# Kernel optimization log

Hardware: AMD Instinct MI355X
Metric: run time of the kernel (lower is better)

The kernel has to match this reference:

```python
import math
import jax, jax.numpy as jnp
import numpy as np

B, L, H = 32, 1024, 128

def setup_inputs() -> dict:
    key = jax.random.key(0)
    k1, k2, k3, k4 = jax.random.split(key, 4)
    a = jax.random.normal(k1, (B, L, H), dtype=jnp.float32)
    b = jax.random.normal(k2, (B, L, H), dtype=jnp.float32)
    mask_a = jax.random.randint(k3, (B, L, 1), 0, 2, dtype=jnp.int32)
    mask_b = jax.random.randint(k4, (B, L, 1), 0, 2, dtype=jnp.int32)
    temperature = jnp.asarray(1.0 / math.sqrt(H), dtype=jnp.float32)
    return {"a": a, "b": b, "mask_a": mask_a, "mask_b": mask_b, "temperature": temperature}

def reference(a, b, mask_a, mask_b, temperature):
    # scores: [B, La, Lb]
    scores = jnp.einsum('bld,bmd->blm', a, b) * temperature
    # outer product of token validity masks -> pair mask [B, La, Lb]
    mask = jnp.einsum('blk,bmk->blm', mask_a.astype(jnp.float32), mask_b.astype(jnp.float32)) > 0
    scores = jnp.where(mask, scores, jnp.float32(-10000.0))
    attention_a = jax.nn.softmax(scores, axis=1)  # normalize over La (columns)
    attention_b = jax.nn.softmax(scores, axis=2)  # normalize over Lb (rows)
    feature_a = jnp.einsum('blm,bmd->bld', attention_b, b)
    feature_b = jnp.einsum('blm,bmd->bld', attention_a, a)  # valid since La == Lb
    return (feature_a, feature_b)
```

## Files before the change

kernel.cpp:

```cpp
#include <hip/hip_runtime.h>
#include <math.h>

#define BN 32
#define LL 1024
#define HH 128

typedef __attribute__((ext_vector_type(8))) short short8;
typedef __attribute__((ext_vector_type(4))) float f32x4;

static const size_t SZ_BF = (size_t)BN * LL * HH * 2;

__device__ __forceinline__ ushort f2bf(float x) {
  union { float f; unsigned u; } c; c.f = x;
  unsigned r = c.u + 0x7fffu + ((c.u >> 16) & 1u);
  return (ushort)(r >> 16);
}
__device__ __forceinline__ float bf2f(ushort h) {
  union { unsigned u; float f; } c; c.u = ((unsigned)h) << 16;
  return c.f;
}
__device__ __forceinline__ short8 ld8(const ushort* p) {
  return *(const short8*)p;
}

__global__ __launch_bounds__(256) void k_convert(
    const float* __restrict__ a, const float* __restrict__ b,
    const int* __restrict__ mask_b,
    ushort* __restrict__ abf, ushort* __restrict__ bbf,
    ushort* __restrict__ aT, ushort* __restrict__ bT,
    float* __restrict__ meanb, float* __restrict__ invmean) {
  int bb = blockIdx.y;
  int l0 = blockIdx.x * 64;
  int which = blockIdx.z;
  const float* src = which ? b : a;
  ushort* dst  = which ? bbf : abf;
  ushort* dstT = which ? bT : aT;
  float* dmean = which ? meanb : invmean;
  __shared__ __align__(16) ushort T[128][72];
  __shared__ float accS[128];
  __shared__ float wgt[64];
  int t = threadIdx.x;
  if (t < 128) accS[t] = 0.f;
  if (t < 64)
    wgt[t] = which ? 1.0f : ((mask_b[bb * LL + l0 + t] == 0) ? 1.0f : 0.0f);
  int lrow = t >> 5;
  int dcol = (t & 31) * 4;
#pragma unroll
  for (int p = 0; p < 8; ++p) {
    int l = p * 8 + lrow;
    float4 v = *(const float4*)&src[((size_t)bb * LL + l0 + l) * HH + dcol];
    ushort4 u;
    u.x = f2bf(v.x); u.y = f2bf(v.y); u.z = f2bf(v.z); u.w = f2bf(v.w);
    *(ushort4*)&dst[((size_t)bb * LL + l0 + l) * HH + dcol] = u;
    T[dcol + 0][l] = u.x; T[dcol + 1][l] = u.y;
    T[dcol + 2][l] = u.z; T[dcol + 3][l] = u.w;
  }
  __syncthreads();
  int drow = t >> 3;
  int c8 = (t & 7) * 8;
#pragma unroll
  for (int q = 0; q < 4; ++q) {
    int d = q * 32 + drow;
    short8 val = *(const short8*)&T[d][c8];
    *(short8*)&dstT[((size_t)bb * HH + d) * LL + l0 + c8] = val;
    float s = 0.f;
#pragma unroll
    for (int j = 0; j < 8; ++j) s += wgt[c8 + j] * bf2f((ushort)val[j]);
    atomicAdd(&accS[d], s);
  }
  __syncthreads();
  if (t < 128) atomicAdd(&dmean[bb * HH + t], accS[t]);
}


__global__ __launch_bounds__(256, 2) void k_colsum(
    const ushort* __restrict__ abf, const ushort* __restrict__ bbf,
    ushort* __restrict__ aTm,
    const int* __restrict__ mask_a, const int* __restrict__ mask_b,
    const float* __restrict__ temp_p, float2* __restrict__ cc) {
  int wg = blockIdx.x;
  int xcd = wg & 7, k_ = wg >> 3;
  int bb = (k_ >> 4) * 8 + xcd;
  int m0 = (k_ & 15) * 64;
  int t = threadIdx.x;
  int w = t >> 6, lane = t & 63, l16 = lane & 15, quad = lane >> 4;
  float temp = temp_p[0];
  __shared__ __align__(16) float biasA[LL];
  __shared__ float csred[4][4][16];
  __shared__ float invS[64];
  for (int i = t; i < LL; i += 256)
    biasA[i] = mask_a[bb * LL + i] ? 0.0f : -10000.0f;

  short8 Bm[4][4];
  float biasB_mt[4];
#pragma unroll
  for (int mt = 0; mt < 4; ++mt) {
    int m = m0 + mt * 16 + l16;
    biasB_mt[mt] = mask_b[bb * LL + m] ? 0.0f : -10000.0f;
#pragma unroll
    for (int k = 0; k < 4; ++k)
      Bm[mt][k] = ld8(&bbf[((size_t)bb * LL + m) * HH + k * 32 + quad * 8]);
  }
  __syncthreads();

  float cs[4] = {0.f, 0.f, 0.f, 0.f};
  short8 Al0[4], Al1[4];

#define LOADAL(AlX, IT)                                                       \
  {                                                                           \
    const ushort* arow = &abf[((size_t)bb * LL + w * 256 + (IT) * 16 + l16) * HH]; \
    _Pragma("unroll") for (int k = 0; k < 4; ++k)                             \
        AlX[k] = ld8(&arow[k * 32 + quad * 8]);                               \
  }

#define CSCOMPUTE(AlX, IT)                                                    \
  {                                                                           \
    int lbase = w * 256 + (IT) * 16;                                          \
    f32x4 bA = *(const f32x4*)&biasA[lbase + quad * 4];                       \
    _Pragma("unroll") for (int mt = 0; mt < 4; ++mt) {                        \
      f32x4 sacc = {0.f, 0.f, 0.f, 0.f};                                      \
      _Pragma("unroll") for (int k = 0; k < 4; ++k)                           \
          sacc = __builtin_amdgcn_mfma_f32_16x16x32_bf16(AlX[k], Bm[mt][k],   \
                                                         sacc, 0, 0, 0);      \
      _Pragma("unroll") for (int r = 0; r < 4; ++r)                           \
          cs[mt] += __expf(sacc[r] * temp + bA[r] + biasB_mt[mt]);            \
    }                                                                         \
  }

  LOADAL(Al0, 0);
  for (int it = 0; it < 16; it += 2) {
    LOADAL(Al1, it + 1);
    CSCOMPUTE(Al0, it);
    LOADAL(Al0, (it + 2) & 15);
    CSCOMPUTE(Al1, it + 1);
  }
#undef LOADAL
#undef CSCOMPUTE

#pragma unroll
  for (int mt = 0; mt < 4; ++mt) {
    cs[mt] += __shfl_xor(cs[mt], 16);
    cs[mt] += __shfl_xor(cs[mt], 32);
  }
  if (lane < 16) {
#pragma unroll
    for (int mt = 0; mt < 4; ++mt) csred[w][mt][l16] = cs[mt];
  }
  __syncthreads();
  if (t < 64) {
    int mt = t >> 4, ml = t & 15;
    float s = csred[0][mt][ml] + csred[1][mt][ml] + csred[2][mt][ml] + csred[3][mt][ml];
    int m = m0 + t;
    float bB = mask_b[bb * LL + m] ? 0.0f : -10000.0f;
    float inv = s > 0.f ? 1.0f / s : 0.0f;
    invS[t] = inv;
    cc[bb * LL + m] = make_float2(inv, bB);
  }
  __syncthreads();

  {
    int d = t >> 1, mc = (t & 1) * 32;
    ushort* ap = &aTm[((size_t)bb * HH + d) * LL + m0 + mc];
    short8 v0 = ld8(ap), v1 = ld8(ap + 8), v2 = ld8(ap + 16), v3 = ld8(ap + 24);
    ushort o[32];
#pragma unroll
    for (int j = 0; j < 8; ++j) {
      o[j]      = f2bf(bf2f((ushort)v0[j]) * invS[mc + j]);
      o[8 + j]  = f2bf(bf2f((ushort)v1[j]) * invS[mc + 8 + j]);
      o[16 + j] = f2bf(bf2f((ushort)v2[j]) * invS[mc + 16 + j]);
      o[24 + j] = f2bf(bf2f((ushort)v3[j]) * invS[mc + 24 + j]);
    }
    *(short8*)ap        = *(short8*)&o[0];
    *(short8*)(ap + 8)  = *(short8*)&o[8];
    *(short8*)(ap + 16) = *(short8*)&o[16];
    *(short8*)(ap + 24) = *(short8*)&o[24];
  }
}

__global__ __launch_bounds__(256, 2) void k_features(
    const ushort* __restrict__ abf, const ushort* __restrict__ bbf,
    const ushort* __restrict__ aT, const ushort* __restrict__ bT,
    const int* __restrict__ mask_a, const float* __restrict__ temp_p,
    const float2* __restrict__ cc, const float* __restrict__ meanb,
    const float* __restrict__ invmean, float* __restrict__ out) {
  int wg = blockIdx.x;
  int xcd = wg & 7, k_ = wg >> 3;
  int bb = (k_ >> 4) * 8 + xcd;
  int l0 = (k_ & 15) * 64;
  int t = threadIdx.x;
  int w = t >> 6, lane = t & 63, l16 = lane & 15, quad = lane >> 4;
  float temp = temp_p[0];

  __shared__ float2 ccs[LL];
  __shared__ __align__(16) ushort Pa[2][64 * 72];
  __shared__ float rspart[4][64];
  __shared__ float rsfin[64];

  for (int i = t; i < LL; i += 256) ccs[i] = cc[bb * LL + i];

  float biasA_lt[4];
  short8 Afix[4][4];
#pragma unroll
  for (int lt = 0; lt < 4; ++lt) {
    int l = l0 + lt * 16 + l16;
    biasA_lt[lt] = mask_a[bb * LL + l] ? 0.0f : -10000.0f;
#pragma unroll
    for (int k = 0; k < 4; ++k)
      Afix[lt][k] = ld8(&abf[((size_t)bb * LL + l) * HH + k * 32 + quad * 8]);
  }

  f32x4 accA[4][2], accB[4][2];
  f32x4 zero = {0.f, 0.f, 0.f, 0.f};
#pragma unroll
  for (int lt = 0; lt < 4; ++lt)
#pragma unroll
    for (int dt = 0; dt < 2; ++dt) { accA[lt][dt] = zero; accB[lt][dt] = zero; }
  float rs_lt[4] = {0.f, 0.f, 0.f, 0.f};
  __syncthreads();

  short8 Am0[4], Am1[4];
  float cv0[4], cv1[4];
  short8 Bb0[2][2], Ba0[2][2], Bb1[2][2], Ba1[2][2];

#define LOADAM(AmX, cvX, M0)                                                  \
  {                                                                           \
    const ushort* brow = &bbf[((size_t)bb * LL + (M0) + w * 16 + l16) * HH];  \
    _Pragma("unroll") for (int k = 0; k < 4; ++k)                             \
        AmX[k] = ld8(&brow[k * 32 + quad * 8]);                               \
    _Pragma("unroll") for (int r = 0; r < 4; ++r)                             \
        cvX[r] = ccs[(M0) + w * 16 + quad * 4 + r].y;                         \
  }

#define LOADBT(BbX, BaX, M0)                                                  \
  {                                                                           \
    _Pragma("unroll") for (int dt = 0; dt < 2; ++dt) {                        \
      const ushort* btrow =                                                   \
          &bT[((size_t)bb * HH + w * 32 + dt * 16 + l16) * LL + (M0)];        \
      const ushort* atrow =                                                   \
          &aT[((size_t)bb * HH + w * 32 + dt * 16 + l16) * LL + (M0)];        \
      _Pragma("unroll") for (int ks = 0; ks < 2; ++ks) {                      \
        BbX[dt][ks] = ld8(&btrow[ks * 32 + quad * 8]);                        \
        BaX[dt][ks] = ld8(&atrow[ks * 32 + quad * 8]);                        \
      }                                                                       \
    }                                                                         \
  }

#define SPHASE(AmX, cvX, PBUFI)                                               \
  {                                                                           \
    ushort* pa = &Pa[PBUFI][0];                                               \
    _Pragma("unroll") for (int lt = 0; lt < 4; ++lt) {                        \
      f32x4 sacc = zero;                                                      \
      _Pragma("unroll") for (int k = 0; k < 4; ++k)                           \
          sacc = __builtin_amdgcn_mfma_f32_16x16x32_bf16(AmX[k], Afix[lt][k], \
                                                         sacc, 0, 0, 0);      \
      ushort pav[4];                                                          \
      _Pragma("unroll") for (int r = 0; r < 4; ++r) {                         \
        float e = __expf(sacc[r] * temp + biasA_lt[lt] + cvX[r]);             \
        pav[r] = f2bf(e);                                                     \
        rs_lt[lt] += bf2f(pav[r]);                                            \
      }                                                                       \
      uint2 ka;                                                               \
      ka.x = (uint)pav[0] | ((uint)pav[1] << 16);                             \
      ka.y = (uint)pav[2] | ((uint)pav[3] << 16);                             \
      int pidx = (lt * 16 + l16) * 72 + w * 16 + quad * 4;                    \
      *(uint2*)&pa[pidx] = ka;                                                \
    }                                                                         \
  }

#define FPHASE(PBUFI, BbX, BaX)                                               \
  {                                                                           \
    const ushort* pa = &Pa[PBUFI][0];                                         \
    _Pragma("unroll") for (int lt = 0; lt < 4; ++lt) {                        \
      _Pragma("unroll") for (int ks = 0; ks < 2; ++ks) {                      \
        int ridx = (lt * 16 + l16) * 72 + ks * 32 + quad * 8;                 \
        short8 PaF = *(const short8*)&pa[ridx];                               \
        _Pragma("unroll") for (int dt = 0; dt < 2; ++dt) {                    \
          accA[lt][dt] = __builtin_amdgcn_mfma_f32_16x16x32_bf16(             \
              PaF, BbX[dt][ks], accA[lt][dt], 0, 0, 0);                       \
          accB[lt][dt] = __builtin_amdgcn_mfma_f32_16x16x32_bf16(             \
              PaF, BaX[dt][ks], accB[lt][dt], 0, 0, 0);                       \
        }                                                                     \
      }                                                                       \
    }                                                                         \
  }

  LOADAM(Am0, cv0, 0);
  LOADBT(Bb0, Ba0, 0);
  LOADAM(Am1, cv1, 64);
  SPHASE(Am0, cv0, 0);
  __syncthreads();

  for (int kk = 0; kk < 7; ++kk) {
    int mA = (2 * kk + 1) * 64;
    LOADBT(Bb1, Ba1, mA);
    LOADAM(Am0, cv0, mA + 64);
    SPHASE(Am1, cv1, 1);
    FPHASE(0, Bb0, Ba0);
    __syncthreads();
    LOADBT(Bb0, Ba0, mA + 64);
    LOADAM(Am1, cv1, mA + 128);
    SPHASE(Am0, cv0, 0);
    FPHASE(1, Bb1, Ba1);
    __syncthreads();
  }

  LOADBT(Bb1, Ba1, 960);
  SPHASE(Am1, cv1, 1);
  FPHASE(0, Bb0, Ba0);
  __syncthreads();
  FPHASE(1, Bb1, Ba1);

#undef LOADAM
#undef LOADBT
#undef SPHASE
#undef FPHASE

#pragma unroll
  for (int lt = 0; lt < 4; ++lt) {
    rs_lt[lt] += __shfl_xor(rs_lt[lt], 16);
    rs_lt[lt] += __shfl_xor(rs_lt[lt], 32);
  }
  if (lane < 16) {
#pragma unroll
    for (int lt = 0; lt < 4; ++lt) rspart[w][lt * 16 + l16] = rs_lt[lt];
  }
  __syncthreads();
  if (t < 64)
    rsfin[t] = rspart[0][t] + rspart[1][t] + rspart[2][t] + rspart[3][t];
  __syncthreads();

  float* outA = out;
  float* outB = out + (size_t)BN * LL * HH;
#pragma unroll
  for (int dt = 0; dt < 2; ++dt) {
    int d = w * 32 + dt * 16 + l16;
    float mb = meanb[bb * HH + d] * (1.0f / 1024.0f);
    float im = invmean[bb * HH + d] * (1.0f / 1024.0f);
#pragma unroll
    for (int lt = 0; lt < 4; ++lt) {
#pragma unroll
      for (int r = 0; r < 4; ++r) {
        int l = lt * 16 + quad * 4 + r;
        float rsv = rsfin[l];
        float fa = (rsv > 0.f) ? accA[lt][dt][r] / rsv : mb;
        float fb = accB[lt][dt][r] + im;
        __builtin_nontemporal_store(fa, &outA[((size_t)bb * LL + l0 + l) * HH + d]);
        __builtin_nontemporal_store(fb, &outB[((size_t)bb * LL + l0 + l) * HH + d]);
      }
    }
  }
}

extern "C" void kernel_launch(void* const* d_in, const int* in_sizes, int n_in,
                              void* d_out, int out_size, void* d_ws, size_t ws_size,
                              hipStream_t stream) {
  const float* a = (const float*)d_in[0];
  const float* b = (const float*)d_in[1];
  const int* mask_a = (const int*)d_in[2];
  const int* mask_b = (const int*)d_in[3];
  const float* temp = (const float*)d_in[4];
  float* out = (float*)d_out;

  char* wsb = (char*)d_ws;
  ushort* abf = (ushort*)(wsb + 0 * SZ_BF);
  ushort* bbf = (ushort*)(wsb + 1 * SZ_BF);
  ushort* aT  = (ushort*)(wsb + 2 * SZ_BF);
  ushort* bT  = (ushort*)(wsb + 3 * SZ_BF);
  float2* cc  = (float2*)(wsb + 4 * SZ_BF);
  float* meanb   = (float*)(wsb + 4 * SZ_BF + (size_t)BN * LL * sizeof(float2));
  float* invmean = meanb + BN * HH;

  hipMemsetAsync(meanb, 0, 2 * BN * HH * sizeof(float), stream);
  k_convert<<<dim3(16, 32, 2), 256, 0, stream>>>(a, b, mask_b, abf, bbf, aT, bT,
                                                 meanb, invmean);
  k_colsum<<<dim3(512), 256, 0, stream>>>(abf, bbf, aT, mask_a, mask_b, temp, cc);
  k_features<<<dim3(512), 256, 0, stream>>>(abf, bbf, aT, bT, mask_a, temp,
                                            cc, meanb, invmean, out);
  (void)in_sizes; (void)n_in; (void)out_size; (void)ws_size;
}
```

Baseline: 203.8 us.

## Pre-swizzle bf16 operands into MFMA fragment-contiguous chunks

```diff
diff --git a/kernel.cpp b/kernel.cpp
--- a/kernel.cpp
+++ b/kernel.cpp
@@ -23,18 +23,25 @@
   return *(const short8*)p;
 }
 
+__device__ __forceinline__ size_t chunkS(int bb, int g, int k) {
+  return (((size_t)bb * 64 + g) * 4 + k) * 512;
+}
+__device__ __forceinline__ size_t chunkT(int bb, int dg, int mb) {
+  return (((size_t)bb * 8 + dg) * 32 + mb) * 512;
+}
+
 __global__ __launch_bounds__(256) void k_convert(
     const float* __restrict__ a, const float* __restrict__ b,
     const int* __restrict__ mask_b,
-    ushort* __restrict__ abf, ushort* __restrict__ bbf,
-    ushort* __restrict__ aT, ushort* __restrict__ bT,
+    ushort* __restrict__ abfs, ushort* __restrict__ bbfs,
+    ushort* __restrict__ aTs, ushort* __restrict__ bTs,
     float* __restrict__ meanb, float* __restrict__ invmean) {
   int bb = blockIdx.y;
   int l0 = blockIdx.x * 64;
   int which = blockIdx.z;
   const float* src = which ? b : a;
-  ushort* dst  = which ? bbf : abf;
-  ushort* dstT = which ? bT : aT;
+  ushort* dstS = which ? bbfs : abfs;
+  ushort* dstT = which ? bTs : aTs;
   float* dmean = which ? meanb : invmean;
   __shared__ __align__(16) ushort T[128][72];
   __shared__ float accS[128];
@@ -51,22 +58,28 @@
     float4 v = *(const float4*)&src[((size_t)bb * LL + l0 + l) * HH + dcol];
     ushort4 u;
     u.x = f2bf(v.x); u.y = f2bf(v.y); u.z = f2bf(v.z); u.w = f2bf(v.w);
-    *(ushort4*)&dst[((size_t)bb * LL + l0 + l) * HH + dcol] = u;
+    int g = (l0 >> 4) + (l >> 4);
+    int k = dcol >> 5, quadc = (dcol >> 3) & 3, j = dcol & 7;
+    *(ushort4*)&dstS[chunkS(bb, g, k) + (size_t)(quadc * 16 + (l & 15)) * 8 + j] = u;
     T[dcol + 0][l] = u.x; T[dcol + 1][l] = u.y;
     T[dcol + 2][l] = u.z; T[dcol + 3][l] = u.w;
   }
   __syncthreads();
-  int drow = t >> 3;
-  int c8 = (t & 7) * 8;
-#pragma unroll
-  for (int q = 0; q < 4; ++q) {
-    int d = q * 32 + drow;
-    short8 val = *(const short8*)&T[d][c8];
-    *(short8*)&dstT[((size_t)bb * HH + d) * LL + l0 + c8] = val;
+#pragma unroll
+  for (int c = 0; c < 4; ++c) {
+    int cid = c * 4 + (t >> 6);
+    int dg = cid >> 1, mloc = cid & 1;
+    int lane = t & 63, l16c = lane & 15, qc = lane >> 4;
+    int row = dg * 16 + l16c, colb = mloc * 32 + qc * 8;
+    uint2 vlo = *(const uint2*)&T[row][colb];
+    uint2 vhi = *(const uint2*)&T[row][colb + 4];
+    union { uint4 u4; short8 s8; ushort us[8]; } cv_;
+    cv_.u4 = make_uint4(vlo.x, vlo.y, vhi.x, vhi.y);
+    *(short8*)&dstT[chunkT(bb, dg, (l0 >> 5) + mloc) + (size_t)lane * 8] = cv_.s8;
     float s = 0.f;
 #pragma unroll
-    for (int j = 0; j < 8; ++j) s += wgt[c8 + j] * bf2f((ushort)val[j]);
-    atomicAdd(&accS[d], s);
+    for (int jj = 0; jj < 8; ++jj) s += wgt[colb + jj] * bf2f(cv_.us[jj]);
+    atomicAdd(&accS[row], s);
   }
   __syncthreads();
   if (t < 128) atomicAdd(&dmean[bb * HH + t], accS[t]);
@@ -74,7 +87,7 @@
 
 
 __global__ __launch_bounds__(256, 2) void k_colsum(
-    const ushort* __restrict__ abf, const ushort* __restrict__ bbf,
+    const ushort* __restrict__ abfs, const ushort* __restrict__ bbfs,
     ushort* __restrict__ aTm,
     const int* __restrict__ mask_a, const int* __restrict__ mask_b,
     const float* __restrict__ temp_p, float2* __restrict__ cc) {
@@ -99,7 +112,7 @@
     biasB_mt[mt] = mask_b[bb * LL + m] ? 0.0f : -10000.0f;
 #pragma unroll
     for (int k = 0; k < 4; ++k)
-      Bm[mt][k] = ld8(&bbf[((size_t)bb * LL + m) * HH + k * 32 + quad * 8]);
+      Bm[mt][k] = ld8(&bbfs[chunkS(bb, (m0 >> 4) + mt, k) + (size_t)lane * 8]);
   }
   __syncthreads();
 
@@ -108,9 +121,8 @@
 
 #define LOADAL(AlX, IT)                                                       \
   {                                                                           \
-    const ushort* arow = &abf[((size_t)bb * LL + w * 256 + (IT) * 16 + l16) * HH]; \
     _Pragma("unroll") for (int k = 0; k < 4; ++k)                             \
-        AlX[k] = ld8(&arow[k * 32 + quad * 8]);                               \
+        AlX[k] = ld8(&abfs[chunkS(bb, w * 16 + (IT), k) + (size_t)lane * 8]); \
   }
 
 #define CSCOMPUTE(AlX, IT)                                                    \
@@ -158,28 +170,24 @@
   }
   __syncthreads();
 
-  {
-    int d = t >> 1, mc = (t & 1) * 32;
-    ushort* ap = &aTm[((size_t)bb * HH + d) * LL + m0 + mc];
-    short8 v0 = ld8(ap), v1 = ld8(ap + 8), v2 = ld8(ap + 16), v3 = ld8(ap + 24);
-    ushort o[32];
-#pragma unroll
-    for (int j = 0; j < 8; ++j) {
-      o[j]      = f2bf(bf2f((ushort)v0[j]) * invS[mc + j]);
-      o[8 + j]  = f2bf(bf2f((ushort)v1[j]) * invS[mc + 8 + j]);
-      o[16 + j] = f2bf(bf2f((ushort)v2[j]) * invS[mc + 16 + j]);
-      o[24 + j] = f2bf(bf2f((ushort)v3[j]) * invS[mc + 24 + j]);
-    }
-    *(short8*)ap        = *(short8*)&o[0];
-    *(short8*)(ap + 8)  = *(short8*)&o[8];
-    *(short8*)(ap + 16) = *(short8*)&o[16];
-    *(short8*)(ap + 24) = *(short8*)&o[24];
+#pragma unroll
+  for (int q = 0; q < 4; ++q) {
+    int cid = q * 4 + (t >> 6);
+    int dg = cid >> 1, mloc = cid & 1;
+    int ln = t & 63;
+    ushort* ap = &aTm[chunkT(bb, dg, (m0 >> 5) + mloc) + (size_t)ln * 8];
+    short8 v = ld8(ap);
+    int mb = mloc * 32 + (ln >> 4) * 8;
+    ushort o[8];
+#pragma unroll
+    for (int j = 0; j < 8; ++j) o[j] = f2bf(bf2f((ushort)v[j]) * invS[mb + j]);
+    *(short8*)ap = *(short8*)&o[0];
   }
 }
 
 __global__ __launch_bounds__(256, 2) void k_features(
-    const ushort* __restrict__ abf, const ushort* __restrict__ bbf,
-    const ushort* __restrict__ aT, const ushort* __restrict__ bT,
+    const ushort* __restrict__ abfs, const ushort* __restrict__ bbfs,
+    const ushort* __restrict__ aTs, const ushort* __restrict__ bTs,
     const int* __restrict__ mask_a, const float* __restrict__ temp_p,
     const float2* __restrict__ cc, const float* __restrict__ meanb,
     const float* __restrict__ invmean, float* __restrict__ out) {
@@ -206,7 +214,7 @@
     biasA_lt[lt] = mask_a[bb * LL + l] ? 0.0f : -10000.0f;
 #pragma unroll
     for (int k = 0; k < 4; ++k)
-      Afix[lt][k] = ld8(&abf[((size_t)bb * LL + l) * HH + k * 32 + quad * 8]);
+      Afix[lt][k] = ld8(&abfs[chunkS(bb, (l0 >> 4) + lt, k) + (size_t)lane * 8]);
   }
 
   f32x4 accA[4][2], accB[4][2];
@@ -224,9 +232,8 @@
 
 #define LOADAM(AmX, cvX, M0)                                                  \
   {                                                                           \
-    const ushort* brow = &bbf[((size_t)bb * LL + (M0) + w * 16 + l16) * HH];  \
     _Pragma("unroll") for (int k = 0; k < 4; ++k)                             \
-        AmX[k] = ld8(&brow[k * 32 + quad * 8]);                               \
+        AmX[k] = ld8(&bbfs[chunkS(bb, ((M0) >> 4) + w, k) + (size_t)lane * 8]); \
     _Pragma("unroll") for (int r = 0; r < 4; ++r)                             \
         cvX[r] = ccs[(M0) + w * 16 + quad * 4 + r].y;                         \
   }
@@ -234,13 +241,10 @@
 #define LOADBT(BbX, BaX, M0)                                                  \
   {                                                                           \
     _Pragma("unroll") for (int dt = 0; dt < 2; ++dt) {                        \
-      const ushort* btrow =                                                   \
-          &bT[((size_t)bb * HH + w * 32 + dt * 16 + l16) * LL + (M0)];        \
-      const ushort* atrow =                                                   \
-          &aT[((size_t)bb * HH + w * 32 + dt * 16 + l16) * LL + (M0)];        \
       _Pragma("unroll") for (int ks = 0; ks < 2; ++ks) {                      \
-        BbX[dt][ks] = ld8(&btrow[ks * 32 + quad * 8]);                        \
-        BaX[dt][ks] = ld8(&atrow[ks * 32 + quad * 8]);                        \
+        size_t cb = chunkT(bb, w * 2 + dt, ((M0) >> 5) + ks) + (size_t)lane * 8; \
+        BbX[dt][ks] = ld8(&bTs[cb]);                                          \
+        BaX[dt][ks] = ld8(&aTs[cb]);                                          \
       }                                                                       \
     }                                                                         \
   }
@@ -362,19 +366,19 @@
   float* out = (float*)d_out;
 
   char* wsb = (char*)d_ws;
-  ushort* abf = (ushort*)(wsb + 0 * SZ_BF);
-  ushort* bbf = (ushort*)(wsb + 1 * SZ_BF);
-  ushort* aT  = (ushort*)(wsb + 2 * SZ_BF);
-  ushort* bT  = (ushort*)(wsb + 3 * SZ_BF);
+  ushort* abfs = (ushort*)(wsb + 0 * SZ_BF);
+  ushort* bbfs = (ushort*)(wsb + 1 * SZ_BF);
+  ushort* aTs  = (ushort*)(wsb + 2 * SZ_BF);
+  ushort* bTs  = (ushort*)(wsb + 3 * SZ_BF);
   float2* cc  = (float2*)(wsb + 4 * SZ_BF);
   float* meanb   = (float*)(wsb + 4 * SZ_BF + (size_t)BN * LL * sizeof(float2));
   float* invmean = meanb + BN * HH;
 
   hipMemsetAsync(meanb, 0, 2 * BN * HH * sizeof(float), stream);
-  k_convert<<<dim3(16, 32, 2), 256, 0, stream>>>(a, b, mask_b, abf, bbf, aT, bT,
-                                                 meanb, invmean);
-  k_colsum<<<dim3(512), 256, 0, stream>>>(abf, bbf, aT, mask_a, mask_b, temp, cc);
-  k_features<<<dim3(512), 256, 0, stream>>>(abf, bbf, aT, bT, mask_a, temp,
+  k_convert<<<dim3(16, 32, 2), 256, 0, stream>>>(a, b, mask_b, abfs, bbfs, aTs,
+                                                 bTs, meanb, invmean);
+  k_colsum<<<dim3(512), 256, 0, stream>>>(abfs, bbfs, aTs, mask_a, mask_b, temp, cc);
+  k_features<<<dim3(512), 256, 0, stream>>>(abfs, bbfs, aTs, bTs, mask_a, temp,
                                             cc, meanb, invmean, out);
   (void)in_sizes; (void)n_in; (void)out_size; (void)ws_size;
 }
```

Result: faster. 167.8 us (median of 2 runs) (-17.7%).
